# Optimization experiments

Hardware: AMD Instinct MI355X
Metric: run time of the kernel (lower is better)

Reference implementation:

```python
import jax, jax.numpy as jnp
import numpy as np

M, N, D, B, LAYERS = 512, 512, 1024, 4096, 16


def setup_inputs() -> dict:
    key = jax.random.key(0)
    ks = jax.random.split(key, 4)
    x = jax.random.normal(ks[0], (M, B), dtype=jnp.float32)
    A = jax.random.normal(ks[1], (M, D), dtype=jnp.float32) / np.float32(np.sqrt(M))
    # fc[k].weight = A.t() + 0.001*randn  -> shape [d, m]
    W = A.T[None] + 0.001 * jax.random.normal(ks[2], (LAYERS, D, M), dtype=jnp.float32)
    Z0 = (1.0 / D) * jax.random.uniform(ks[3], (D, B), dtype=jnp.float32)
    E0 = jnp.zeros((M, B), dtype=jnp.float32)
    L0 = jnp.zeros((M, B), dtype=jnp.float32)
    ones = jnp.ones((LAYERS,), dtype=jnp.float32)
    return {
        'x': x, 'A': A, 'W': W, 'Z0': Z0, 'E0': E0, 'L0': L0,
        'beta1': ones, 'beta2': ones, 'beta3': ones, 'ss2': ones,
        'active_para': 0.2 * ones, 'active_para1': 0.8 * ones,
    }


def _soft(v, t):
    # self_active: relu(v - t) - relu(-v - t)  (soft threshold)
    return jax.nn.relu(v - t) - jax.nn.relu(-v - t)


def reference(x, A, W, Z0, E0, L0, beta1, beta2, beta3, ss2, active_para, active_para1):
    K = W.shape[0]
    # k = 0 (learned branch)
    T0 = A @ Z0 + E0 - x                      # [m, B]
    Var0 = L0 + beta1[0] * T0
    Z1 = _soft(Z0 - W[0] @ Var0, active_para[0])  # [d, B]

    def step(carry, params):
        Zp, Ep, Lp = carry
        b1, b2, b3, s2, ap, ap1, Wk = params
        AZ = A @ Zp                            # [m, B]
        VVar = Lp + b2 * (AZ + Ep - x)
        En = _soft(Ep - s2 * VVar, ap1)
        Tn = AZ + En - x
        Ln = Lp + b3 * Tn
        Varn = Ln + b1 * Tn
        Zn = _soft(Zp - Wk @ Varn, ap)
        return (Zn, En, Ln), (Zn, En, Ln)

    params = (beta1[1:], beta2[:K - 1], beta3[:K - 1], ss2[:K - 1],
              active_para[1:], active_para1[:K - 1], W[1:])
    _, (Zs, Es, Ls) = jax.lax.scan(step, (Z1, E0, L0), params)
    Z_all = jnp.concatenate([Z1[None], Zs], axis=0)   # [K, d, B]
    E_all = jnp.concatenate([E0[None], Es], axis=0)   # [K, m, B]
    L_all = jnp.concatenate([L0[None], Ls], axis=0)   # [K, m, B]
    return Z_all, E_all, L_all
```

## Files before the change

kernel.cpp:

```cpp
#include <hip/hip_runtime.h>
#include <cstddef>

#define MDIM 512
#define DDIM 1024
#define BDIM 4096
#define NLAYERS 16

constexpr int BK = 16;

__device__ __forceinline__ float softf(float v, float t) {
  return copysignf(fmaxf(fabsf(v) - t, 0.0f), v);
}

template <int MODE, int K, int BN>
__global__ __launch_bounds__(256) void gemm_f32(
    const float* __restrict__ P, const float* __restrict__ Bm,
    const float* __restrict__ xg, const float* __restrict__ Ep,
    const float* __restrict__ Lp, const float* __restrict__ Zp,
    const float* __restrict__ beta1, const float* __restrict__ beta2,
    const float* __restrict__ beta3, const float* __restrict__ ss2,
    const float* __restrict__ apar, const float* __restrict__ apar1, int k,
    float* __restrict__ O0, float* __restrict__ O1, float* __restrict__ O2) {
  constexpr int TN = BN / 16;
  constexpr int NG = BN / 64;
  __shared__ __align__(16) float As[2][BK][68];
  __shared__ __align__(16) float Bs[2][BK][BN];

  const int tid = threadIdx.x;
  const int tn = tid & 15, tm = tid >> 4;
  const int m0 = blockIdx.x * 64, n0 = blockIdx.y * BN;

  float acc[4][TN];
#pragma unroll
  for (int r = 0; r < 4; ++r)
#pragma unroll
    for (int c = 0; c < TN; ++c) acc[r][c] = 0.0f;

  const int ar = tid >> 2, akc = tid & 3;
  const float* gA = P + (size_t)(m0 + ar) * K + akc * 4;
  const int br = (NG == 1) ? (tid >> 4) : (tid >> 5);
  const int bc = (NG == 1) ? (tid & 15) : (tid & 31);
  const float* gB = Bm + (size_t)br * BDIM + n0 + bc * 4;

  float4 ra, rb0, rb1;
  auto gload = [&](int k0) {
    ra = *reinterpret_cast<const float4*>(gA + (size_t)k0);
    rb0 = *reinterpret_cast<const float4*>(gB + (size_t)k0 * BDIM);
    if (NG == 2)
      rb1 = *reinterpret_cast<const float4*>(gB + (size_t)(k0 + 8) * BDIM);
  };
  auto stagewr = [&](int bb) {
    As[bb][akc * 4 + 0][ar] = ra.x;
    As[bb][akc * 4 + 1][ar] = ra.y;
    As[bb][akc * 4 + 2][ar] = ra.z;
    As[bb][akc * 4 + 3][ar] = ra.w;
    *reinterpret_cast<float4*>(&Bs[bb][br][bc * 4]) = rb0;
    if (NG == 2) *reinterpret_cast<float4*>(&Bs[bb][br + 8][bc * 4]) = rb1;
  };
  auto comp = [&](int bb) {
#pragma unroll
    for (int kk = 0; kk < BK; ++kk) {
      const float4 a4 = *reinterpret_cast<const float4*>(&As[bb][kk][tm * 4]);
      const float a[4] = {a4.x, a4.y, a4.z, a4.w};
      float bv[TN];
#pragma unroll
      for (int g = 0; g < NG; ++g)
        *reinterpret_cast<float4*>(&bv[g * 4]) =
            *reinterpret_cast<const float4*>(&Bs[bb][kk][g * 64 + tn * 4]);
#pragma unroll
      for (int r = 0; r < 4; ++r)
#pragma unroll
        for (int c = 0; c < TN; ++c) acc[r][c] = fmaf(a[r], bv[c], acc[r][c]);
    }
  };

  constexpr int NS = K / BK;
  gload(0);
  stagewr(0);
  __syncthreads();
  int bb = 0;
#pragma unroll 1
  for (int t = 1; t < NS; ++t) {
    gload(t * BK);
    comp(bb);
    stagewr(bb ^ 1);
    __syncthreads();
    bb ^= 1;
  }
  comp(bb);

  const float b1v = (MODE == 2) ? 0.f : beta1[k];
  float b2v = 0.f, b3v = 0.f, s2v = 0.f, a1v = 0.f, ap = 0.f;
  if (MODE == 1) {
    b2v = beta2[k - 1];
    b3v = beta3[k - 1];
    s2v = ss2[k - 1];
    a1v = apar1[k - 1];
  }
  if (MODE == 2) ap = apar[k];

#pragma unroll
  for (int r = 0; r < 4; ++r) {
    const int row = m0 + tm * 4 + r;
#pragma unroll
    for (int g = 0; g < NG; ++g) {
      const int col = n0 + g * 64 + tn * 4;
      const size_t off = (size_t)row * BDIM + col;
      if (MODE == 2) {
        const float4 z4 = *reinterpret_cast<const float4*>(&Zp[off]);
        const float z[4] = {z4.x, z4.y, z4.z, z4.w};
        float4 o;
        float* op = reinterpret_cast<float*>(&o);
#pragma unroll
        for (int j = 0; j < 4; ++j)
          op[j] = softf(z[j] - acc[r][g * 4 + j], ap);
        *reinterpret_cast<float4*>(&O0[off]) = o;
      } else {
        float ev[4], lv[4], xv[4];
        *reinterpret_cast<float4*>(&ev[0]) =
            *reinterpret_cast<const float4*>(&Ep[off]);
        *reinterpret_cast<float4*>(&lv[0]) =
            *reinterpret_cast<const float4*>(&Lp[off]);
        *reinterpret_cast<float4*>(&xv[0]) =
            *reinterpret_cast<const float4*>(&xg[off]);
        float vo[4], eo[4], lo_[4];
#pragma unroll
        for (int j = 0; j < 4; ++j) {
          const float az = acc[r][g * 4 + j];
          if (MODE == 0) {
            const float t0 = az + ev[j] - xv[j];
            vo[j] = fmaf(b1v, t0, lv[j]);
            eo[j] = ev[j];
            lo_[j] = lv[j];
          } else {
            const float vv = fmaf(b2v, az + ev[j] - xv[j], lv[j]);
            const float en = softf(ev[j] - s2v * vv, a1v);
            const float tn_ = az + en - xv[j];
            const float ln = fmaf(b3v, tn_, lv[j]);
            eo[j] = en;
            lo_[j] = ln;
            vo[j] = fmaf(b1v, tn_, ln);
          }
        }
        *reinterpret_cast<float4*>(&O0[off]) =
            *reinterpret_cast<const float4*>(&vo[0]);
        *reinterpret_cast<float4*>(&O1[off]) =
            *reinterpret_cast<const float4*>(&eo[0]);
        *reinterpret_cast<float4*>(&O2[off]) =
            *reinterpret_cast<const float4*>(&lo_[0]);
      }
    }
  }
}

extern "C" void kernel_launch(void* const* d_in, const int* in_sizes, int n_in,
                              void* d_out, int out_size, void* d_ws,
                              size_t ws_size, hipStream_t stream) {
  (void)in_sizes;
  (void)n_in;
  (void)out_size;
  (void)ws_size;
  const float* x = (const float*)d_in[0];
  const float* A = (const float*)d_in[1];
  const float* W = (const float*)d_in[2];
  const float* Z0 = (const float*)d_in[3];
  const float* E0 = (const float*)d_in[4];
  const float* L0 = (const float*)d_in[5];
  const float* beta1 = (const float*)d_in[6];
  const float* beta2 = (const float*)d_in[7];
  const float* beta3 = (const float*)d_in[8];
  const float* ss2 = (const float*)d_in[9];
  const float* apar = (const float*)d_in[10];
  const float* apar1 = (const float*)d_in[11];

  constexpr size_t DB = (size_t)DDIM * BDIM;
  constexpr size_t MB = (size_t)MDIM * BDIM;
  float* Zall = (float*)d_out;
  float* Eall = Zall + (size_t)NLAYERS * DB;
  float* Lall = Eall + (size_t)NLAYERS * MB;
  float* Var = (float*)d_ws;

  const dim3 blk(256);
  const dim3 gA(MDIM / 64, BDIM / 64);
  const dim3 gB(DDIM / 64, BDIM / 128);

  gemm_f32<0, DDIM, 64><<<gA, blk, 0, stream>>>(
      A, Z0, x, E0, L0, nullptr, beta1, beta2, beta3, ss2, apar, apar1, 0, Var,
      Eall, Lall);
  gemm_f32<2, MDIM, 128><<<gB, blk, 0, stream>>>(
      W, Var, nullptr, nullptr, nullptr, Z0, beta1, beta2, beta3, ss2, apar,
      apar1, 0, Zall, nullptr, nullptr);
  for (int k = 1; k < NLAYERS; ++k) {
    const float* Zp = Zall + (size_t)(k - 1) * DB;
    gemm_f32<1, DDIM, 64><<<gA, blk, 0, stream>>>(
        A, Zp, x, Eall + (size_t)(k - 1) * MB, Lall + (size_t)(k - 1) * MB,
        nullptr, beta1, beta2, beta3, ss2, apar, apar1, k,
        Var, Eall + (size_t)k * MB, Lall + (size_t)k * MB);
    gemm_f32<2, MDIM, 128><<<gB, blk, 0, stream>>>(
        W + (size_t)k * DDIM * MDIM, Var, nullptr, nullptr, nullptr, Zp, beta1,
        beta2, beta3, ss2, apar, apar1, k, Zall + (size_t)k * DB, nullptr,
        nullptr);
  }
}
```

Before: 2.052 ms.

## Replace LDS-tiled GEMM with register-resident wavefront GEMM using scalar A loads

```diff
diff --git a/kernel.cpp b/kernel.cpp
--- a/kernel.cpp
+++ b/kernel.cpp
@@ -6,14 +6,12 @@
 #define BDIM 4096
 #define NLAYERS 16
 
-constexpr int BK = 16;
-
 __device__ __forceinline__ float softf(float v, float t) {
   return copysignf(fmaxf(fabsf(v) - t, 0.0f), v);
 }
 
-template <int MODE, int K, int BN>
-__global__ __launch_bounds__(256) void gemm_f32(
+template <int MODE, int K, int TM>
+__global__ __launch_bounds__(256) void gemm_rr(
     const float* __restrict__ P, const float* __restrict__ Bm,
     const float* __restrict__ xg, const float* __restrict__ Ep,
     const float* __restrict__ Lp, const float* __restrict__ Zp,
@@ -21,73 +19,58 @@
     const float* __restrict__ beta3, const float* __restrict__ ss2,
     const float* __restrict__ apar, const float* __restrict__ apar1, int k,
     float* __restrict__ O0, float* __restrict__ O1, float* __restrict__ O2) {
-  constexpr int TN = BN / 16;
-  constexpr int NG = BN / 64;
-  __shared__ __align__(16) float As[2][BK][68];
-  __shared__ __align__(16) float Bs[2][BK][BN];
+  const int lane = threadIdx.x & 63;
+  const int w = __builtin_amdgcn_readfirstlane((int)(threadIdx.x >> 6));
+  const int r0 = blockIdx.x * (4 * TM) + w * TM;
+  const int c0 = blockIdx.y * 256 + lane * 4;
 
-  const int tid = threadIdx.x;
-  const int tn = tid & 15, tm = tid >> 4;
-  const int m0 = blockIdx.x * 64, n0 = blockIdx.y * BN;
+  const float* pA = P + (size_t)r0 * K;
+  const float* pB = Bm + c0;
 
-  float acc[4][TN];
+  float acc[TM][4];
 #pragma unroll
-  for (int r = 0; r < 4; ++r)
+  for (int r = 0; r < TM; ++r)
 #pragma unroll
-    for (int c = 0; c < TN; ++c) acc[r][c] = 0.0f;
+    for (int c = 0; c < 4; ++c) acc[r][c] = 0.0f;
 
-  const int ar = tid >> 2, akc = tid & 3;
-  const float* gA = P + (size_t)(m0 + ar) * K + akc * 4;
-  const int br = (NG == 1) ? (tid >> 4) : (tid >> 5);
-  const int bc = (NG == 1) ? (tid & 15) : (tid & 31);
-  const float* gB = Bm + (size_t)br * BDIM + n0 + bc * 4;
+  float4 b0[8], b1[8];
 
-  float4 ra, rb0, rb1;
-  auto gload = [&](int k0) {
-    ra = *reinterpret_cast<const float4*>(gA + (size_t)k0);
-    rb0 = *reinterpret_cast<const float4*>(gB + (size_t)k0 * BDIM);
-    if (NG == 2)
-      rb1 = *reinterpret_cast<const float4*>(gB + (size_t)(k0 + 8) * BDIM);
+  auto loadB = [&](float4 (&bb)[8], int kc) {
+    const float* base = pB + (size_t)kc * 8 * BDIM;
+#pragma unroll
+    for (int j = 0; j < 8; ++j)
+      bb[j] = *reinterpret_cast<const float4*>(base + (size_t)j * BDIM);
   };
-  auto stagewr = [&](int bb) {
-    As[bb][akc * 4 + 0][ar] = ra.x;
-    As[bb][akc * 4 + 1][ar] = ra.y;
-    As[bb][akc * 4 + 2][ar] = ra.z;
-    As[bb][akc * 4 + 3][ar] = ra.w;
-    *reinterpret_cast<float4*>(&Bs[bb][br][bc * 4]) = rb0;
-    if (NG == 2) *reinterpret_cast<float4*>(&Bs[bb][br + 8][bc * 4]) = rb1;
-  };
-  auto comp = [&](int bb) {
+
+  auto compute = [&](const float4 (&bb)[8], int kc) {
 #pragma unroll
-    for (int kk = 0; kk < BK; ++kk) {
-      const float4 a4 = *reinterpret_cast<const float4*>(&As[bb][kk][tm * 4]);
-      const float a[4] = {a4.x, a4.y, a4.z, a4.w};
-      float bv[TN];
+    for (int r = 0; r < TM; ++r) {
+      const float* aR = pA + (size_t)r * K + kc * 8;
+      float a[8];
 #pragma unroll
-      for (int g = 0; g < NG; ++g)
-        *reinterpret_cast<float4*>(&bv[g * 4]) =
-            *reinterpret_cast<const float4*>(&Bs[bb][kk][g * 64 + tn * 4]);
+      for (int j = 0; j < 8; ++j) a[j] = aR[j];
 #pragma unroll
-      for (int r = 0; r < 4; ++r)
-#pragma unroll
-        for (int c = 0; c < TN; ++c) acc[r][c] = fmaf(a[r], bv[c], acc[r][c]);
+      for (int j = 0; j < 8; ++j) {
+        acc[r][0] = fmaf(a[j], bb[j].x, acc[r][0]);
+        acc[r][1] = fmaf(a[j], bb[j].y, acc[r][1]);
+        acc[r][2] = fmaf(a[j], bb[j].z, acc[r][2]);
+        acc[r][3] = fmaf(a[j], bb[j].w, acc[r][3]);
+      }
     }
   };
 
-  constexpr int NS = K / BK;
-  gload(0);
-  stagewr(0);
-  __syncthreads();
-  int bb = 0;
+  constexpr int NC = K / 8;
+  loadB(b0, 0);
 #pragma unroll 1
-  for (int t = 1; t < NS; ++t) {
-    gload(t * BK);
-    comp(bb);
-    stagewr(bb ^ 1);
-    __syncthreads();
-    bb ^= 1;
+  for (int kc = 0; kc + 2 < NC; kc += 2) {
+    loadB(b1, kc + 1);
+    compute(b0, kc);
+    loadB(b0, kc + 2);
+    compute(b1, kc + 1);
   }
-  comp(bb);
+  loadB(b1, NC - 1);
+  compute(b0, NC - 2);
+  compute(b1, NC - 1);
 
   const float b1v = (MODE == 2) ? 0.f : beta1[k];
   float b2v = 0.f, b3v = 0.f, s2v = 0.f, a1v = 0.f, ap = 0.f;
@@ -100,55 +83,49 @@
   if (MODE == 2) ap = apar[k];
 
 #pragma unroll
-  for (int r = 0; r < 4; ++r) {
-    const int row = m0 + tm * 4 + r;
+  for (int r = 0; r < TM; ++r) {
+    const size_t off = (size_t)(r0 + r) * BDIM + c0;
+    if (MODE == 2) {
+      const float4 z4 = *reinterpret_cast<const float4*>(&Zp[off]);
+      const float z[4] = {z4.x, z4.y, z4.z, z4.w};
+      float o[4];
 #pragma unroll
-    for (int g = 0; g < NG; ++g) {
-      const int col = n0 + g * 64 + tn * 4;
-      const size_t off = (size_t)row * BDIM + col;
-      if (MODE == 2) {
-        const float4 z4 = *reinterpret_cast<const float4*>(&Zp[off]);
-        const float z[4] = {z4.x, z4.y, z4.z, z4.w};
-        float4 o;
-        float* op = reinterpret_cast<float*>(&o);
+      for (int j = 0; j < 4; ++j) o[j] = softf(z[j] - acc[r][j], ap);
+      *reinterpret_cast<float4*>(&O0[off]) =
+          *reinterpret_cast<const float4*>(&o[0]);
+    } else {
+      float ev[4], lv[4], xv[4];
+      *reinterpret_cast<float4*>(&ev[0]) =
+          *reinterpret_cast<const float4*>(&Ep[off]);
+      *reinterpret_cast<float4*>(&lv[0]) =
+          *reinterpret_cast<const float4*>(&Lp[off]);
+      *reinterpret_cast<float4*>(&xv[0]) =
+          *reinterpret_cast<const float4*>(&xg[off]);
+      float vo[4], eo[4], lo_[4];
 #pragma unroll
-        for (int j = 0; j < 4; ++j)
-          op[j] = softf(z[j] - acc[r][g * 4 + j], ap);
-        *reinterpret_cast<float4*>(&O0[off]) = o;
-      } else {
-        float ev[4], lv[4], xv[4];
-        *reinterpret_cast<float4*>(&ev[0]) =
-            *reinterpret_cast<const float4*>(&Ep[off]);
-        *reinterpret_cast<float4*>(&lv[0]) =
-            *reinterpret_cast<const float4*>(&Lp[off]);
-        *reinterpret_cast<float4*>(&xv[0]) =
-            *reinterpret_cast<const float4*>(&xg[off]);
-        float vo[4], eo[4], lo_[4];
-#pragma unroll
-        for (int j = 0; j < 4; ++j) {
-          const float az = acc[r][g * 4 + j];
-          if (MODE == 0) {
-            const float t0 = az + ev[j] - xv[j];
-            vo[j] = fmaf(b1v, t0, lv[j]);
-            eo[j] = ev[j];
-            lo_[j] = lv[j];
-          } else {
-            const float vv = fmaf(b2v, az + ev[j] - xv[j], lv[j]);
-            const float en = softf(ev[j] - s2v * vv, a1v);
-            const float tn_ = az + en - xv[j];
-            const float ln = fmaf(b3v, tn_, lv[j]);
-            eo[j] = en;
-            lo_[j] = ln;
-            vo[j] = fmaf(b1v, tn_, ln);
-          }
+      for (int j = 0; j < 4; ++j) {
+        const float az = acc[r][j];
+        if (MODE == 0) {
+          const float t0 = az + ev[j] - xv[j];
+          vo[j] = fmaf(b1v, t0, lv[j]);
+          eo[j] = ev[j];
+          lo_[j] = lv[j];
+        } else {
+          const float vv = fmaf(b2v, az + ev[j] - xv[j], lv[j]);
+          const float en = softf(ev[j] - s2v * vv, a1v);
+          const float tn_ = az + en - xv[j];
+          const float ln = fmaf(b3v, tn_, lv[j]);
+          eo[j] = en;
+          lo_[j] = ln;
+          vo[j] = fmaf(b1v, tn_, ln);
         }
-        *reinterpret_cast<float4*>(&O0[off]) =
-            *reinterpret_cast<const float4*>(&vo[0]);
-        *reinterpret_cast<float4*>(&O1[off]) =
-            *reinterpret_cast<const float4*>(&eo[0]);
-        *reinterpret_cast<float4*>(&O2[off]) =
-            *reinterpret_cast<const float4*>(&lo_[0]);
       }
+      *reinterpret_cast<float4*>(&O0[off]) =
+          *reinterpret_cast<const float4*>(&vo[0]);
+      *reinterpret_cast<float4*>(&O1[off]) =
+          *reinterpret_cast<const float4*>(&eo[0]);
+      *reinterpret_cast<float4*>(&O2[off]) =
+          *reinterpret_cast<const float4*>(&lo_[0]);
     }
   }
 }
@@ -181,22 +158,22 @@
   float* Var = (float*)d_ws;
 
   const dim3 blk(256);
-  const dim3 gA(MDIM / 64, BDIM / 64);
-  const dim3 gB(DDIM / 64, BDIM / 128);
+  const dim3 gA(MDIM / 16, BDIM / 256);
+  const dim3 gB(DDIM / 32, BDIM / 256);
 
-  gemm_f32<0, DDIM, 64><<<gA, blk, 0, stream>>>(
+  gemm_rr<0, DDIM, 4><<<gA, blk, 0, stream>>>(
       A, Z0, x, E0, L0, nullptr, beta1, beta2, beta3, ss2, apar, apar1, 0, Var,
       Eall, Lall);
-  gemm_f32<2, MDIM, 128><<<gB, blk, 0, stream>>>(
+  gemm_rr<2, MDIM, 8><<<gB, blk, 0, stream>>>(
       W, Var, nullptr, nullptr, nullptr, Z0, beta1, beta2, beta3, ss2, apar,
       apar1, 0, Zall, nullptr, nullptr);
   for (int k = 1; k < NLAYERS; ++k) {
     const float* Zp = Zall + (size_t)(k - 1) * DB;
-    gemm_f32<1, DDIM, 64><<<gA, blk, 0, stream>>>(
+    gemm_rr<1, DDIM, 4><<<gA, blk, 0, stream>>>(
         A, Zp, x, Eall + (size_t)(k - 1) * MB, Lall + (size_t)(k - 1) * MB,
-        nullptr, beta1, beta2, beta3, ss2, apar, apar1, k,
-        Var, Eall + (size_t)k * MB, Lall + (size_t)k * MB);
-    gemm_f32<2, MDIM, 128><<<gB, blk, 0, stream>>>(
+        nullptr, beta1, beta2, beta3, ss2, apar, apar1, k, Var,
+        Eall + (size_t)k * MB, Lall + (size_t)k * MB);
+    gemm_rr<2, MDIM, 8><<<gB, blk, 0, stream>>>(
         W + (size_t)k * DDIM * MDIM, Var, nullptr, nullptr, nullptr, Zp, beta1,
         beta2, beta3, ss2, apar, apar1, k, Zall + (size_t)k * DB, nullptr,
         nullptr);
```

Result: slower. 2.612 ms (+27.3%).

## Retile fp32 GEMMs to 32x128 blocks with wave-uniform row broadcasts

Applied to the files above, without the earlier changes.

```diff
diff --git a/kernel.cpp b/kernel.cpp
--- a/kernel.cpp
+++ b/kernel.cpp
@@ -12,8 +12,8 @@
   return copysignf(fmaxf(fabsf(v) - t, 0.0f), v);
 }
 
-template <int MODE, int K, int BN>
-__global__ __launch_bounds__(256) void gemm_f32(
+template <int MODE, int K>
+__global__ __launch_bounds__(256) void gemm_bc(
     const float* __restrict__ P, const float* __restrict__ Bm,
     const float* __restrict__ xg, const float* __restrict__ Ep,
     const float* __restrict__ Lp, const float* __restrict__ Zp,
@@ -21,56 +21,54 @@
     const float* __restrict__ beta3, const float* __restrict__ ss2,
     const float* __restrict__ apar, const float* __restrict__ apar1, int k,
     float* __restrict__ O0, float* __restrict__ O1, float* __restrict__ O2) {
-  constexpr int TN = BN / 16;
-  constexpr int NG = BN / 64;
-  __shared__ __align__(16) float As[2][BK][68];
-  __shared__ __align__(16) float Bs[2][BK][BN];
+  __shared__ __align__(16) float As[2][BK][32];
+  __shared__ __align__(16) float Bs[2][BK][128];
 
   const int tid = threadIdx.x;
-  const int tn = tid & 15, tm = tid >> 4;
-  const int m0 = blockIdx.x * 64, n0 = blockIdx.y * BN;
+  const int lane = tid & 63;
+  const int w = __builtin_amdgcn_readfirstlane((int)(tid >> 6));
+  const int m0 = blockIdx.x * 32, n0 = blockIdx.y * 128;
+  const int r0 = m0 + w * 8;
+  const int c0 = n0 + lane * 2;
 
-  float acc[4][TN];
+  float acc[8][2];
 #pragma unroll
-  for (int r = 0; r < 4; ++r)
-#pragma unroll
-    for (int c = 0; c < TN; ++c) acc[r][c] = 0.0f;
+  for (int r = 0; r < 8; ++r) {
+    acc[r][0] = 0.0f;
+    acc[r][1] = 0.0f;
+  }
 
-  const int ar = tid >> 2, akc = tid & 3;
-  const float* gA = P + (size_t)(m0 + ar) * K + akc * 4;
-  const int br = (NG == 1) ? (tid >> 4) : (tid >> 5);
-  const int bc = (NG == 1) ? (tid & 15) : (tid & 31);
-  const float* gB = Bm + (size_t)br * BDIM + n0 + bc * 4;
+  const int ar = tid >> 3, akc = (tid & 7) * 2;
+  const float* gA = P + (size_t)(m0 + ar) * K + akc;
+  const int br = tid >> 4, bc = (tid & 15) * 8;
+  const float* gB = Bm + (size_t)br * BDIM + n0 + bc;
 
-  float4 ra, rb0, rb1;
+  float2 rA;
+  float4 rB0, rB1;
   auto gload = [&](int k0) {
-    ra = *reinterpret_cast<const float4*>(gA + (size_t)k0);
-    rb0 = *reinterpret_cast<const float4*>(gB + (size_t)k0 * BDIM);
-    if (NG == 2)
-      rb1 = *reinterpret_cast<const float4*>(gB + (size_t)(k0 + 8) * BDIM);
+    rA = *reinterpret_cast<const float2*>(gA + (size_t)k0);
+    rB0 = *reinterpret_cast<const float4*>(gB + (size_t)k0 * BDIM);
+    rB1 = *reinterpret_cast<const float4*>(gB + (size_t)k0 * BDIM + 4);
   };
   auto stagewr = [&](int bb) {
-    As[bb][akc * 4 + 0][ar] = ra.x;
-    As[bb][akc * 4 + 1][ar] = ra.y;
-    As[bb][akc * 4 + 2][ar] = ra.z;
-    As[bb][akc * 4 + 3][ar] = ra.w;
-    *reinterpret_cast<float4*>(&Bs[bb][br][bc * 4]) = rb0;
-    if (NG == 2) *reinterpret_cast<float4*>(&Bs[bb][br + 8][bc * 4]) = rb1;
+    As[bb][akc][ar] = rA.x;
+    As[bb][akc + 1][ar] = rA.y;
+    *reinterpret_cast<float4*>(&Bs[bb][br][bc]) = rB0;
+    *reinterpret_cast<float4*>(&Bs[bb][br][bc + 4]) = rB1;
   };
   auto comp = [&](int bb) {
 #pragma unroll
     for (int kk = 0; kk < BK; ++kk) {
-      const float4 a4 = *reinterpret_cast<const float4*>(&As[bb][kk][tm * 4]);
-      const float a[4] = {a4.x, a4.y, a4.z, a4.w};
-      float bv[TN];
+      const float4 a0 = *reinterpret_cast<const float4*>(&As[bb][kk][w * 8]);
+      const float4 a1 =
+          *reinterpret_cast<const float4*>(&As[bb][kk][w * 8 + 4]);
+      const float a[8] = {a0.x, a0.y, a0.z, a0.w, a1.x, a1.y, a1.z, a1.w};
+      const float2 b2 = *reinterpret_cast<const float2*>(&Bs[bb][kk][lane * 2]);
 #pragma unroll
-      for (int g = 0; g < NG; ++g)
-        *reinterpret_cast<float4*>(&bv[g * 4]) =
-            *reinterpret_cast<const float4*>(&Bs[bb][kk][g * 64 + tn * 4]);
-#pragma unroll
-      for (int r = 0; r < 4; ++r)
-#pragma unroll
-        for (int c = 0; c < TN; ++c) acc[r][c] = fmaf(a[r], bv[c], acc[r][c]);
+      for (int r = 0; r < 8; ++r) {
+        acc[r][0] = fmaf(a[r], b2.x, acc[r][0]);
+        acc[r][1] = fmaf(a[r], b2.y, acc[r][1]);
+      }
     }
   };
 
@@ -100,55 +98,50 @@
   if (MODE == 2) ap = apar[k];
 
 #pragma unroll
-  for (int r = 0; r < 4; ++r) {
-    const int row = m0 + tm * 4 + r;
+  for (int r = 0; r < 8; ++r) {
+    const size_t off = (size_t)(r0 + r) * BDIM + c0;
+    if (MODE == 2) {
+      const float2 z2 = *reinterpret_cast<const float2*>(&Zp[off]);
+      float2 o;
+      o.x = softf(z2.x - acc[r][0], ap);
+      o.y = softf(z2.y - acc[r][1], ap);
+      *reinterpret_cast<float2*>(&O0[off]) = o;
+    } else {
+      const float2 e2 = *reinterpret_cast<const float2*>(&Ep[off]);
+      const float2 l2 = *reinterpret_cast<const float2*>(&Lp[off]);
+      const float2 x2 = *reinterpret_cast<const float2*>(&xg[off]);
+      const float ev[2] = {e2.x, e2.y};
+      const float lv[2] = {l2.x, l2.y};
+      const float xv[2] = {x2.x, x2.y};
+      float vo[2], eo[2], lo_[2];
 #pragma unroll
-    for (int g = 0; g < NG; ++g) {
-      const int col = n0 + g * 64 + tn * 4;
-      const size_t off = (size_t)row * BDIM + col;
-      if (MODE == 2) {
-        const float4 z4 = *reinterpret_cast<const float4*>(&Zp[off]);
-        const float z[4] = {z4.x, z4.y, z4.z, z4.w};
-        float4 o;
-        float* op = reinterpret_cast<float*>(&o);
-#pragma unroll
-        for (int j = 0; j < 4; ++j)
-          op[j] = softf(z[j] - acc[r][g * 4 + j], ap);
-        *reinterpret_cast<float4*>(&O0[off]) = o;
-      } else {
-        float ev[4], lv[4], xv[4];
-        *reinterpret_cast<float4*>(&ev[0]) =
-            *reinterpret_cast<const float4*>(&Ep[off]);
-        *reinterpret_cast<float4*>(&lv[0]) =
-            *reinterpret_cast<const float4*>(&Lp[off]);
-        *reinterpret_cast<float4*>(&xv[0]) =
-            *reinterpret_cast<const float4*>(&xg[off]);
-        float vo[4], eo[4], lo_[4];
-#pragma unroll
-        for (int j = 0; j < 4; ++j) {
-          const float az = acc[r][g * 4 + j];
-          if (MODE == 0) {
-            const float t0 = az + ev[j] - xv[j];
-            vo[j] = fmaf(b1v, t0, lv[j]);
-            eo[j] = ev[j];
-            lo_[j] = lv[j];
-          } else {
-            const float vv = fmaf(b2v, az + ev[j] - xv[j], lv[j]);
-            const float en = softf(ev[j] - s2v * vv, a1v);
-            const float tn_ = az + en - xv[j];
-            const float ln = fmaf(b3v, tn_, lv[j]);
-            eo[j] = en;
-            lo_[j] = ln;
-            vo[j] = fmaf(b1v, tn_, ln);
-          }
+      for (int j = 0; j < 2; ++j) {
+        const float az = acc[r][j];
+        if (MODE == 0) {
+          const float t0 = az + ev[j] - xv[j];
+          vo[j] = fmaf(b1v, t0, lv[j]);
+          eo[j] = ev[j];
+          lo_[j] = lv[j];
+        } else {
+          const float vv = fmaf(b2v, az + ev[j] - xv[j], lv[j]);
+          const float en = softf(ev[j] - s2v * vv, a1v);
+          const float tn_ = az + en - xv[j];
+          const float ln = fmaf(b3v, tn_, lv[j]);
+          eo[j] = en;
+          lo_[j] = ln;
+          vo[j] = fmaf(b1v, tn_, ln);
         }
-        *reinterpret_cast<float4*>(&O0[off]) =
-            *reinterpret_cast<const float4*>(&vo[0]);
-        *reinterpret_cast<float4*>(&O1[off]) =
-            *reinterpret_cast<const float4*>(&eo[0]);
-        *reinterpret_cast<float4*>(&O2[off]) =
-            *reinterpret_cast<const float4*>(&lo_[0]);
       }
+      float2 t2;
+      t2.x = vo[0];
+      t2.y = vo[1];
+      *reinterpret_cast<float2*>(&O0[off]) = t2;
+      t2.x = eo[0];
+      t2.y = eo[1];
+      *reinterpret_cast<float2*>(&O1[off]) = t2;
+      t2.x = lo_[0];
+      t2.y = lo_[1];
+      *reinterpret_cast<float2*>(&O2[off]) = t2;
     }
   }
 }
@@ -181,22 +174,22 @@
   float* Var = (float*)d_ws;
 
   const dim3 blk(256);
-  const dim3 gA(MDIM / 64, BDIM / 64);
-  const dim3 gB(DDIM / 64, BDIM / 128);
+  const dim3 gA(MDIM / 32, BDIM / 128);
+  const dim3 gB(DDIM / 32, BDIM / 128);
 
-  gemm_f32<0, DDIM, 64><<<gA, blk, 0, stream>>>(
+  gemm_bc<0, DDIM><<<gA, blk, 0, stream>>>(
       A, Z0, x, E0, L0, nullptr, beta1, beta2, beta3, ss2, apar, apar1, 0, Var,
       Eall, Lall);
-  gemm_f32<2, MDIM, 128><<<gB, blk, 0, stream>>>(
+  gemm_bc<2, MDIM><<<gB, blk, 0, stream>>>(
       W, Var, nullptr, nullptr, nullptr, Z0, beta1, beta2, beta3, ss2, apar,
       apar1, 0, Zall, nullptr, nullptr);
   for (int k = 1; k < NLAYERS; ++k) {
     const float* Zp = Zall + (size_t)(k - 1) * DB;
-    gemm_f32<1, DDIM, 64><<<gA, blk, 0, stream>>>(
+    gemm_bc<1, DDIM><<<gA, blk, 0, stream>>>(
         A, Zp, x, Eall + (size_t)(k - 1) * MB, Lall + (size_t)(k - 1) * MB,
-        nullptr, beta1, beta2, beta3, ss2, apar, apar1, k,
-        Var, Eall + (size_t)k * MB, Lall + (size_t)k * MB);
-    gemm_f32<2, MDIM, 128><<<gB, blk, 0, stream>>>(
+        nullptr, beta1, beta2, beta3, ss2, apar, apar1, k, Var,
+        Eall + (size_t)k * MB, Lall + (size_t)k * MB);
+    gemm_bc<2, MDIM><<<gB, blk, 0, stream>>>(
         W + (size_t)k * DDIM * MDIM, Var, nullptr, nullptr, nullptr, Zp, beta1,
         beta2, beta3, ss2, apar, apar1, k, Zall + (size_t)k * DB, nullptr,
         nullptr);
```

Result: slower. 2.445 ms (+19.1%).
